# Optimization experiments

Hardware: AMD Instinct MI355X
Metric: run time of the kernel (lower is better)

Reference implementation:

```python
import jax, jax.numpy as jnp
import numpy as np

BETA = 0.9
THRESHOLD = 1.0

B, T, I, H, O = 64, 512, 256, 512, 256


def setup_inputs() -> dict:
    key = jax.random.key(0)
    ks = jax.random.split(key, 10)
    s_in = 1.0 / np.sqrt(I)
    s_h = 1.0 / np.sqrt(H)
    return {
        "x": jax.random.normal(ks[0], (B, T, I), dtype=jnp.float32),
        "W_in": jax.random.uniform(ks[1], (H, I), jnp.float32, -s_in, s_in),
        "b_in": jax.random.uniform(ks[2], (H,), jnp.float32, -s_in, s_in),
        "W_ih": jax.random.uniform(ks[3], (H, H), jnp.float32, -s_h, s_h),
        "b_ih": jax.random.uniform(ks[4], (H,), jnp.float32, -s_h, s_h),
        "W_hh": jax.random.uniform(ks[5], (H, H), jnp.float32, -s_h, s_h),
        "b_hh": jax.random.uniform(ks[6], (H,), jnp.float32, -s_h, s_h),
        "W_out": jax.random.uniform(ks[7], (O, H), jnp.float32, -s_h, s_h),
        "b_out": jax.random.uniform(ks[8], (O,), jnp.float32, -s_h, s_h),
        "temporal_attention": jax.random.normal(ks[9], (T, O), dtype=jnp.float32),
    }


def _lif(mem, cur):
    # LIF with 'subtract' reset: new_mem*(1-s) + s*(new_mem-thr) == new_mem - s*thr
    new_mem = BETA * mem + cur
    spike = (new_mem > THRESHOLD).astype(new_mem.dtype)
    return new_mem - spike * THRESHOLD, spike


def reference(x, W_in, b_in, W_ih, b_ih, W_hh, b_hh, W_out, b_out, temporal_attention):
    dtype = x.dtype
    batch, time_steps, _ = x.shape
    hidden = W_in.shape[0]

    # Input projection for all time steps at once: (B,T,H) -> scan over T.
    input_proj = jnp.einsum('bti,hi->tbh', x, W_in) + b_in  # (T,B,H)

    mem0 = jnp.zeros((batch, hidden), dtype=dtype)
    _, hidden_spikes = jax.lax.scan(_lif, mem0, input_proj)  # (T,B,H)

    # Recurrent layer: input->hidden projection precomputed; hidden->hidden uses
    # carried membrane potential (as in the torch module).
    in_proj = jnp.einsum('tbh,gh->tbg', hidden_spikes, W_ih) + b_ih  # (T,B,H)

    def rec_step(mem, ip):
        total = ip + mem @ W_hh.T + b_hh
        return _lif(mem, total)

    _, temporal_spikes = jax.lax.scan(rec_step, mem0, in_proj)  # (T,B,H)

    out_proj = jnp.einsum('tbh,oh->tbo', temporal_spikes, W_out) + b_out  # (T,B,O)

    attn = jax.nn.softmax(temporal_attention[:time_steps], axis=0)  # (T,O)
    attended = jnp.einsum('tbo,to->bo', out_proj, attn)  # (B,O)

    # Final LIF from zero membrane: new_mem = attended; spike = (attended > thr)
    final_spikes = (attended > THRESHOLD).astype(dtype)
    return final_spikes
```

## Files before the change

### kernel.cpp

```cpp
#include <hip/hip_runtime.h>
#include <hip/hip_bf16.h>
#include <cstdint>


#define T_STEPS 512
#define BATCH 64
#define HID 512
#define IN_DIM 256
#define OUT_DIM 256
#define BETA 0.9f
#define THR 1.0f
#define SENT 0x7FC00000u

typedef __attribute__((ext_vector_type(8))) short short8;
typedef __attribute__((ext_vector_type(4))) float float4v;
typedef unsigned short ushort_t;

__global__ __launch_bounds__(256) void k_fill_nan(uint32_t* __restrict__ P) {
  const int idx = blockIdx.x * 256 + threadIdx.x;
  uint4 s = make_uint4(SENT, SENT, SENT, SENT);
  uint4* p4 = (uint4*)P;
  for (int i = idx; i < (32768 * 512) / 4; i += 65536) p4[i] = s;
}

__global__ __launch_bounds__(256) void k_split(const float* __restrict__ src,
                                               ushort_t* __restrict__ hi,
                                               ushort_t* __restrict__ lo, int n) {
  int i = blockIdx.x * 256 + threadIdx.x;
  const int stride = gridDim.x * 256;
  for (; i < n; i += stride) {
    float v = src[i];
    uint32_t u = __float_as_uint(v);
    uint32_t rh = u + 0x7FFFu + ((u >> 16) & 1u);
    ushort_t h = (ushort_t)(rh >> 16);
    float hf = __uint_as_float(((uint32_t)h) << 16);
    float l = v - hf;
    uint32_t ul = __float_as_uint(l);
    uint32_t rl = ul + 0x7FFFu + ((ul >> 16) & 1u);
    hi[i] = h;
    lo[i] = (ushort_t)(rl >> 16);
  }
}

__global__ __launch_bounds__(256) void k_softmax_t(
    const float* __restrict__ TA, float* __restrict__ attn) {
  __shared__ float redm[8][32];
  __shared__ float reds[8][32];
  const int ol = threadIdx.x & 31;
  const int tg = threadIdx.x >> 5;
  const int o = blockIdx.x * 32 + ol;
  float mx = -1e30f;
  for (int i = 0; i < 64; ++i) {
    float v = TA[(size_t)(tg * 64 + i) * OUT_DIM + o];
    mx = fmaxf(mx, v);
  }
  redm[tg][ol] = mx;
  __syncthreads();
  float m = redm[0][ol];
#pragma unroll
  for (int j = 1; j < 8; ++j) m = fmaxf(m, redm[j][ol]);
  float s = 0.f;
  for (int i = 0; i < 64; ++i) {
    float v = TA[(size_t)(tg * 64 + i) * OUT_DIM + o];
    s += __expf(v - m);
  }
  reds[tg][ol] = s;
  __syncthreads();
  float tot = 0.f;
#pragma unroll
  for (int j = 0; j < 8; ++j) tot += reds[j][ol];
  const float inv = 1.0f / tot;
  for (int i = 0; i < 64; ++i) {
    int t = tg * 64 + i;
    float v = TA[(size_t)t * OUT_DIM + o];
    attn[(size_t)t * OUT_DIM + o] = __expf(v - m) * inv;
  }
}

__global__ __launch_bounds__(256) void k_gemm_split3(
    const ushort_t* __restrict__ Ahi, const ushort_t* __restrict__ Alo,
    const ushort_t* __restrict__ Bhi, const ushort_t* __restrict__ Blo,
    const float* __restrict__ bias, float* __restrict__ C,
    int M, int N, int K) {
  __shared__ ushort_t At[2][128 * 40];
  __shared__ ushort_t Bt[2][128 * 40];
  const int tid = threadIdx.x;
  const int row0 = blockIdx.x * 128, col0 = blockIdx.y * 128;
  const int w = tid >> 6, lane = tid & 63;
  const int wm = (w >> 1) * 64, wn = (w & 1) * 64;
  const int l15 = lane & 15, quad = lane >> 4;
  float4v acc[4][4];
#pragma unroll
  for (int i = 0; i < 4; ++i)
#pragma unroll
    for (int j = 0; j < 4; ++j) acc[i][j] = (float4v){0.f, 0.f, 0.f, 0.f};

  for (int k0 = 0; k0 < K; k0 += 32) {
#pragma unroll
    for (int it = 0; it < 2; ++it) {
      int idx = it * 256 + tid;
      int r = idx >> 2;
      int c8 = (idx & 3) << 3;
      *(uint4*)(&At[0][r * 40 + c8]) =
          *(const uint4*)(&Ahi[(size_t)(row0 + r) * K + k0 + c8]);
      *(uint4*)(&At[1][r * 40 + c8]) =
          *(const uint4*)(&Alo[(size_t)(row0 + r) * K + k0 + c8]);
      *(uint4*)(&Bt[0][r * 40 + c8]) =
          *(const uint4*)(&Bhi[(size_t)(col0 + r) * K + k0 + c8]);
      *(uint4*)(&Bt[1][r * 40 + c8]) =
          *(const uint4*)(&Blo[(size_t)(col0 + r) * K + k0 + c8]);
    }
    __syncthreads();
    short8 ah[4], al[4], bh[4], bl[4];
    const int koff = quad * 8;
#pragma unroll
    for (int i = 0; i < 4; ++i) {
      ah[i] = *(const short8*)(&At[0][(wm + i * 16 + l15) * 40 + koff]);
      al[i] = *(const short8*)(&At[1][(wm + i * 16 + l15) * 40 + koff]);
      bh[i] = *(const short8*)(&Bt[0][(wn + i * 16 + l15) * 40 + koff]);
      bl[i] = *(const short8*)(&Bt[1][(wn + i * 16 + l15) * 40 + koff]);
    }
#pragma unroll
    for (int i = 0; i < 4; ++i)
#pragma unroll
      for (int j = 0; j < 4; ++j) {
        acc[i][j] = __builtin_amdgcn_mfma_f32_16x16x32_bf16(ah[i], bh[j], acc[i][j], 0, 0, 0);
        acc[i][j] = __builtin_amdgcn_mfma_f32_16x16x32_bf16(ah[i], bl[j], acc[i][j], 0, 0, 0);
        acc[i][j] = __builtin_amdgcn_mfma_f32_16x16x32_bf16(al[i], bh[j], acc[i][j], 0, 0, 0);
      }
    __syncthreads();
  }
#pragma unroll
  for (int j = 0; j < 4; ++j) {
    const int col = col0 + wn + j * 16 + l15;
    const float bv = bias ? bias[col] : 0.f;
#pragma unroll
    for (int i = 0; i < 4; ++i) {
#pragma unroll
      for (int r = 0; r < 4; ++r) {
        int row = row0 + wm + i * 16 + quad * 4 + r;
        C[(size_t)row * N + col] = acc[i][j][r] + bv;
      }
    }
  }
}

__global__ __launch_bounds__(256) void k_gemm_spike2(
    const float* __restrict__ A, const ushort_t* __restrict__ Bhi,
    const ushort_t* __restrict__ Blo, const float* __restrict__ bias,
    float* __restrict__ C, int M, int N, int K) {
  __shared__ ushort_t At[128 * 72];
  __shared__ ushort_t Bt[2][128 * 72];
  const int tid = threadIdx.x;
  const int row0 = blockIdx.x * 128, col0 = blockIdx.y * 128;
  const int w = tid >> 6, lane = tid & 63;
  const int wm = (w >> 1) * 64, wn = (w & 1) * 64;
  const int l15 = lane & 15, quad = lane >> 4;
  float4v acc[4][4];
#pragma unroll
  for (int i = 0; i < 4; ++i)
#pragma unroll
    for (int j = 0; j < 4; ++j) acc[i][j] = (float4v){0.f, 0.f, 0.f, 0.f};

  for (int k0 = 0; k0 < K; k0 += 64) {
#pragma unroll
    for (int it = 0; it < 4; ++it) {
      int idx = it * 256 + tid;
      int r = idx >> 3;
      int c8 = (idx & 7) << 3;
      uint4 pa = *(const uint4*)(&A[(size_t)(row0 + r) * K + k0 + c8]);
      uint4 pb = *(const uint4*)(&A[(size_t)(row0 + r) * K + k0 + c8 + 4]);
      uint4 st;
      st.x = (pa.x >> 16) | (pa.y & 0xFFFF0000u);
      st.y = (pa.z >> 16) | (pa.w & 0xFFFF0000u);
      st.z = (pb.x >> 16) | (pb.y & 0xFFFF0000u);
      st.w = (pb.z >> 16) | (pb.w & 0xFFFF0000u);
      *(uint4*)(&At[r * 72 + c8]) = st;
      *(uint4*)(&Bt[0][r * 72 + c8]) =
          *(const uint4*)(&Bhi[(size_t)(col0 + r) * K + k0 + c8]);
      *(uint4*)(&Bt[1][r * 72 + c8]) =
          *(const uint4*)(&Blo[(size_t)(col0 + r) * K + k0 + c8]);
    }
    __syncthreads();
#pragma unroll
    for (int ks = 0; ks < 2; ++ks) {
      short8 a[4], bh[4], bl[4];
      const int koff = ks * 32 + quad * 8;
#pragma unroll
      for (int i = 0; i < 4; ++i) {
        a[i] = *(const short8*)(&At[(wm + i * 16 + l15) * 72 + koff]);
        bh[i] = *(const short8*)(&Bt[0][(wn + i * 16 + l15) * 72 + koff]);
        bl[i] = *(const short8*)(&Bt[1][(wn + i * 16 + l15) * 72 + koff]);
      }
#pragma unroll
      for (int i = 0; i < 4; ++i)
#pragma unroll
        for (int j = 0; j < 4; ++j) {
          acc[i][j] = __builtin_amdgcn_mfma_f32_16x16x32_bf16(a[i], bh[j], acc[i][j], 0, 0, 0);
          acc[i][j] = __builtin_amdgcn_mfma_f32_16x16x32_bf16(a[i], bl[j], acc[i][j], 0, 0, 0);
        }
    }
    __syncthreads();
  }
#pragma unroll
  for (int j = 0; j < 4; ++j) {
    const int col = col0 + wn + j * 16 + l15;
    const float bv = bias ? bias[col] : 0.f;
#pragma unroll
    for (int i = 0; i < 4; ++i) {
#pragma unroll
      for (int r = 0; r < 4; ++r) {
        int row = row0 + wm + i * 16 + quad * 4 + r;
        C[(size_t)row * N + col] = acc[i][j][r] + bv;
      }
    }
  }
}

__global__ __launch_bounds__(256) void k_lif1(float* __restrict__ p) {
  const int id = blockIdx.x * 256 + threadIdx.x;
  const size_t base = (size_t)(id >> 9) * (T_STEPS * HID) + (id & 511);
  float mem = 0.f;
  for (int t0 = 0; t0 < T_STEPS; t0 += 8) {
    float v[8];
#pragma unroll
    for (int j = 0; j < 8; ++j) v[j] = p[base + (size_t)(t0 + j) * HID];
#pragma unroll
    for (int j = 0; j < 8; ++j) {
      float nm = BETA * mem + v[j];
      float sp = nm > THR ? 1.0f : 0.0f;
      p[base + (size_t)(t0 + j) * HID] = sp;
      mem = nm - sp;
    }
  }
}

__global__ __launch_bounds__(512) void k_recurrent_cp(
    const float* __restrict__ W, const float* __restrict__ b_hh,
    float* __restrict__ rp, float* __restrict__ P) {
  const int tid = threadIdx.x;
  const int grp = blockIdx.x & 31;
  const int j   = blockIdx.x >> 5;
  const int w   = tid >> 6;
  const int l   = tid & 63;
  const int q   = l >> 3;
  const int c   = l & 7;
  const int row = (w << 3) + q;
  const int g0  = j << 6;

  __shared__ float memLDS[2][2][8 * 72];

  for (int i = tid; i < 2 * 2 * 8 * 72; i += 512) ((float*)memLDS)[i] = 0.f;

  float Wreg[64];
  {
    const float* wrow = W + (size_t)(g0 + row) * HID + (c << 6);
#pragma unroll
    for (int k4 = 0; k4 < 16; ++k4) {
      float4 w4 = *(const float4*)(wrow + 4 * k4);
      Wreg[4 * k4 + 0] = w4.x; Wreg[4 * k4 + 1] = w4.y;
      Wreg[4 * k4 + 2] = w4.z; Wreg[4 * k4 + 3] = w4.w;
    }
  }

  const bool lif = (c == 0);
  const int og = g0 + row;
  const size_t rp_b0 = (size_t)(grp * 2 + 0) * (T_STEPS * HID) + og;
  const size_t rp_b1 = (size_t)(grp * 2 + 1) * (T_STEPS * HID) + og;
  const float bhh_v = lif ? b_hh[og] : 0.f;
  float mem0 = 0.f, mem1 = 0.f;

  const int rg = (tid < g0) ? tid : tid + 64;
  const int raddr = (rg >> 6) * 72 + (rg & 63);

  const uint32_t* Pu = (const uint32_t*)P;
  float* Pf = P;

  __syncthreads();

  for (int t = 0; t < T_STEPS; ++t) {
    const int par = t & 1;
    float ip0 = 0.f, ip1 = 0.f;
    if (lif) {
      ip0 = rp[rp_b0 + (size_t)t * HID];
      ip1 = rp[rp_b1 + (size_t)t * HID];
    }
    if (t > 0 && tid < 448) {
      const size_t slot = ((size_t)(t - 1) * 32 + grp) * 1024;
      const uint32_t* a0p = Pu + slot + rg;
      const uint32_t* a1p = a0p + 512;
      uint32_t u0 = __hip_atomic_load(a0p, __ATOMIC_RELAXED, __HIP_MEMORY_SCOPE_AGENT);
      uint32_t u1 = __hip_atomic_load(a1p, __ATOMIC_RELAXED, __HIP_MEMORY_SCOPE_AGENT);
      if (u0 == SENT || u1 == SENT) {
        uint32_t v0 = __hip_atomic_load(a0p, __ATOMIC_RELAXED, __HIP_MEMORY_SCOPE_AGENT);
        uint32_t v1 = __hip_atomic_load(a1p, __ATOMIC_RELAXED, __HIP_MEMORY_SCOPE_AGENT);
        int tries = 0;
        do {
          uint32_t w0 = __hip_atomic_load(a0p, __ATOMIC_RELAXED, __HIP_MEMORY_SCOPE_AGENT);
          uint32_t w1 = __hip_atomic_load(a1p, __ATOMIC_RELAXED, __HIP_MEMORY_SCOPE_AGENT);
          if (u0 == SENT) u0 = v0;
          if (u1 == SENT) u1 = v1;
          v0 = w0; v1 = w1;
          if (++tries > 24) __builtin_amdgcn_s_sleep(1);
        } while (u0 == SENT || u1 == SENT);
      }
      memLDS[par][0][raddr] = __uint_as_float(u0);
      memLDS[par][1][raddr] = __uint_as_float(u1);
    }
    __syncthreads();

    float p0a = 0.f, p0b = 0.f, p1a = 0.f, p1b = 0.f;
    {
      const float4* m0 = (const float4*)&memLDS[par][0][c * 72];
      const float4* m1 = (const float4*)&memLDS[par][1][c * 72];
#pragma unroll
      for (int k4 = 0; k4 < 16; ++k4) {
        float4 a = m0[k4];
        float4 b = m1[k4];
        p0a = fmaf(Wreg[4 * k4 + 0], a.x, p0a);
        p0b = fmaf(Wreg[4 * k4 + 1], a.y, p0b);
        p0a = fmaf(Wreg[4 * k4 + 2], a.z, p0a);
        p0b = fmaf(Wreg[4 * k4 + 3], a.w, p0b);
        p1a = fmaf(Wreg[4 * k4 + 0], b.x, p1a);
        p1b = fmaf(Wreg[4 * k4 + 1], b.y, p1b);
        p1a = fmaf(Wreg[4 * k4 + 2], b.z, p1a);
        p1b = fmaf(Wreg[4 * k4 + 3], b.w, p1b);
      }
    }
    const int i0 = __float_as_int(p0a + p0b);
    const int i1 = __float_as_int(p1a + p1b);
    float s0 = 0.f, s1 = 0.f;
#define RED(ss)                                                                 \
    s0 += __int_as_float(__builtin_amdgcn_ds_swizzle(i0, ((ss) << 5) | 0x18)); \
    s1 += __int_as_float(__builtin_amdgcn_ds_swizzle(i1, ((ss) << 5) | 0x18));
    RED(0) RED(1) RED(2) RED(3) RED(4) RED(5) RED(6) RED(7)
#undef RED

    if (lif) {
      const int npar = par ^ 1;
      const size_t slot = ((size_t)t * 32 + grp) * 1024;
      const float nm0 = BETA * mem0 + ip0 + s0 + bhh_v;
      const float sp0 = nm0 > THR ? 1.0f : 0.0f;
      mem0 = nm0 - sp0;
      __hip_atomic_store(Pf + slot + og, mem0, __ATOMIC_RELAXED, __HIP_MEMORY_SCOPE_AGENT);
      const float nm1 = BETA * mem1 + ip1 + s1 + bhh_v;
      const float sp1 = nm1 > THR ? 1.0f : 0.0f;
      mem1 = nm1 - sp1;
      __hip_atomic_store(Pf + slot + 512 + og, mem1, __ATOMIC_RELAXED, __HIP_MEMORY_SCOPE_AGENT);
      rp[rp_b0 + (size_t)t * HID] = sp0;
      rp[rp_b1 + (size_t)t * HID] = sp1;
      memLDS[npar][0][j * 72 + row] = mem0;
      memLDS[npar][1][j * 72 + row] = mem1;
    }
  }
}

__global__ __launch_bounds__(256) void k_attend(
    const float* __restrict__ op, const float* __restrict__ attn,
    const float* __restrict__ b_out, float* __restrict__ out) {
  const int b = blockIdx.x;
  const int o = threadIdx.x;
  float s = b_out[o];
  const float* opb = op + (size_t)b * T_STEPS * OUT_DIM + o;
  for (int t0 = 0; t0 < T_STEPS; t0 += 8) {
    float av[8], pv[8];
#pragma unroll
    for (int j = 0; j < 8; ++j) {
      av[j] = attn[(size_t)(t0 + j) * OUT_DIM + o];
      pv[j] = opb[(size_t)(t0 + j) * OUT_DIM];
    }
#pragma unroll
    for (int j = 0; j < 8; ++j) s = fmaf(av[j], pv[j], s);
  }
  out[b * OUT_DIM + o] = s > THR ? 1.0f : 0.0f;
}

extern "C" void kernel_launch(void* const* d_in, const int* in_sizes, int n_in,
                              void* d_out, int out_size, void* d_ws, size_t ws_size,
                              hipStream_t stream) {
  (void)in_sizes; (void)n_in; (void)out_size; (void)ws_size;
  const float* x     = (const float*)d_in[0];
  const float* W_in  = (const float*)d_in[1];
  const float* b_in  = (const float*)d_in[2];
  const float* W_ih  = (const float*)d_in[3];
  const float* b_ih  = (const float*)d_in[4];
  const float* W_hh  = (const float*)d_in[5];
  const float* b_hh  = (const float*)d_in[6];
  const float* W_out = (const float*)d_in[7];
  const float* b_out = (const float*)d_in[8];
  const float* TA    = (const float*)d_in[9];

  float* ws = (float*)d_ws;
  float* proj  = ws;
  float* rproj = proj + (size_t)32768 * 512;
  float* attn  = rproj + (size_t)32768 * 512;
  ushort_t* wih_hi = (ushort_t*)(attn + 512 * 256);
  ushort_t* wih_lo = wih_hi + 512 * 512;
  ushort_t* win_hi = wih_lo + 512 * 512;
  ushort_t* win_lo = win_hi + 512 * 256;
  ushort_t* wout_hi = win_lo + 512 * 256;
  ushort_t* wout_lo = wout_hi + 256 * 512;
  ushort_t* x_hi = (ushort_t*)rproj;
  ushort_t* x_lo = x_hi + (size_t)32768 * 256;
  float* P = proj;
  float* out_proj = proj;

  k_softmax_t<<<8, 256, 0, stream>>>(TA, attn);
  k_split<<<4096, 256, 0, stream>>>(x, x_hi, x_lo, 32768 * 256);
  k_split<<<512, 256, 0, stream>>>(W_in, win_hi, win_lo, 512 * 256);
  k_split<<<512, 256, 0, stream>>>(W_ih, wih_hi, wih_lo, 512 * 512);
  k_split<<<512, 256, 0, stream>>>(W_out, wout_hi, wout_lo, 256 * 512);

  k_gemm_split3<<<dim3(256, 4), 256, 0, stream>>>(
      x_hi, x_lo, win_hi, win_lo, b_in, proj, 32768, 512, 256);
  k_lif1<<<128, 256, 0, stream>>>(proj);
  k_gemm_spike2<<<dim3(256, 4), 256, 0, stream>>>(
      proj, wih_hi, wih_lo, b_ih, rproj, 32768, 512, 512);
  k_fill_nan<<<256, 256, 0, stream>>>((uint32_t*)P);
  k_recurrent_cp<<<256, 512, 0, stream>>>(W_hh, b_hh, rproj, P);
  k_gemm_spike2<<<dim3(256, 2), 256, 0, stream>>>(
      rproj, wout_hi, wout_lo, nullptr, out_proj, 32768, 256, 512);
  k_attend<<<64, 256, 0, stream>>>(out_proj, attn, b_out, (float*)d_out);
}
```

Baseline: 1.049 ms.

## Give each wave a private LDS copy of memory state and drop block barriers

Each wavefront now loads the full previous-step membrane vector for both batches itself and keeps it in its own LDS slice. This removes the per-timestep __syncthreads and the block-local LDS forwarding. The two batch values are packed into one 64-bit word, so one atomic store and one atomic load carry a pair. The cost is roughly 8x more global loads per block per step, with every wave polling sentinels independently, in exchange for no block-wide barrier on the serial critical path.

```diff
diff --git a/kernel.cpp b/kernel.cpp
--- a/kernel.cpp
+++ b/kernel.cpp
@@ -248,9 +248,11 @@
   const int row = (w << 3) + q;
   const int g0  = j << 6;
 
-  __shared__ float memLDS[2][2][8 * 72];
-
-  for (int i = tid; i < 2 * 2 * 8 * 72; i += 512) ((float*)memLDS)[i] = 0.f;
+  __shared__ float memLDS[8][2][8 * 72];
+  float* wl0 = &memLDS[w][0][0];
+  float* wl1 = &memLDS[w][1][0];
+
+  for (int i = l; i < 2 * 8 * 72; i += 64) ((float*)memLDS[w])[i] = 0.f;
 
   float Wreg[64];
   {
@@ -270,49 +272,49 @@
   const float bhh_v = lif ? b_hh[og] : 0.f;
   float mem0 = 0.f, mem1 = 0.f;
 
-  const int rg = (tid < g0) ? tid : tid + 64;
-  const int raddr = (rg >> 6) * 72 + (rg & 63);
-
-  const uint32_t* Pu = (const uint32_t*)P;
-  float* Pf = P;
-
-  __syncthreads();
+  const uint64_t* P64 = (const uint64_t*)P;
+  uint64_t* P64w = (uint64_t*)P;
 
   for (int t = 0; t < T_STEPS; ++t) {
-    const int par = t & 1;
     float ip0 = 0.f, ip1 = 0.f;
     if (lif) {
       ip0 = rp[rp_b0 + (size_t)t * HID];
       ip1 = rp[rp_b1 + (size_t)t * HID];
     }
-    if (t > 0 && tid < 448) {
-      const size_t slot = ((size_t)(t - 1) * 32 + grp) * 1024;
-      const uint32_t* a0p = Pu + slot + rg;
-      const uint32_t* a1p = a0p + 512;
-      uint32_t u0 = __hip_atomic_load(a0p, __ATOMIC_RELAXED, __HIP_MEMORY_SCOPE_AGENT);
-      uint32_t u1 = __hip_atomic_load(a1p, __ATOMIC_RELAXED, __HIP_MEMORY_SCOPE_AGENT);
-      if (u0 == SENT || u1 == SENT) {
-        uint32_t v0 = __hip_atomic_load(a0p, __ATOMIC_RELAXED, __HIP_MEMORY_SCOPE_AGENT);
-        uint32_t v1 = __hip_atomic_load(a1p, __ATOMIC_RELAXED, __HIP_MEMORY_SCOPE_AGENT);
-        int tries = 0;
-        do {
-          uint32_t w0 = __hip_atomic_load(a0p, __ATOMIC_RELAXED, __HIP_MEMORY_SCOPE_AGENT);
-          uint32_t w1 = __hip_atomic_load(a1p, __ATOMIC_RELAXED, __HIP_MEMORY_SCOPE_AGENT);
-          if (u0 == SENT) u0 = v0;
-          if (u1 == SENT) u1 = v1;
-          v0 = w0; v1 = w1;
-          if (++tries > 24) __builtin_amdgcn_s_sleep(1);
-        } while (u0 == SENT || u1 == SENT);
-      }
-      memLDS[par][0][raddr] = __uint_as_float(u0);
-      memLDS[par][1][raddr] = __uint_as_float(u1);
-    }
-    __syncthreads();
+    if (t > 0) {
+      const uint64_t* base = P64 + ((size_t)(t - 1) * 32 + grp) * 512;
+      uint64_t u[8];
+#pragma unroll
+      for (int i = 0; i < 8; ++i)
+        u[i] = __hip_atomic_load(base + (i << 6) + l, __ATOMIC_RELAXED,
+                                 __HIP_MEMORY_SCOPE_AGENT);
+      int tries = 0;
+      for (;;) {
+        bool any = false;
+#pragma unroll
+        for (int i = 0; i < 8; ++i) {
+          any = any || ((uint32_t)u[i] == SENT) || ((uint32_t)(u[i] >> 32) == SENT);
+        }
+        if (!any) break;
+        if (++tries > 16) __builtin_amdgcn_s_sleep(1);
+#pragma unroll
+        for (int i = 0; i < 8; ++i) {
+          if (((uint32_t)u[i] == SENT) || ((uint32_t)(u[i] >> 32) == SENT))
+            u[i] = __hip_atomic_load(base + (i << 6) + l, __ATOMIC_RELAXED,
+                                     __HIP_MEMORY_SCOPE_AGENT);
+        }
+      }
+#pragma unroll
+      for (int i = 0; i < 8; ++i) {
+        wl0[i * 72 + l] = __uint_as_float((uint32_t)u[i]);
+        wl1[i * 72 + l] = __uint_as_float((uint32_t)(u[i] >> 32));
+      }
+    }
 
     float p0a = 0.f, p0b = 0.f, p1a = 0.f, p1b = 0.f;
     {
-      const float4* m0 = (const float4*)&memLDS[par][0][c * 72];
-      const float4* m1 = (const float4*)&memLDS[par][1][c * 72];
+      const float4* m0 = (const float4*)&wl0[c * 72];
+      const float4* m1 = (const float4*)&wl1[c * 72];
 #pragma unroll
       for (int k4 = 0; k4 < 16; ++k4) {
         float4 a = m0[k4];
@@ -337,20 +339,18 @@
 #undef RED
 
     if (lif) {
-      const int npar = par ^ 1;
-      const size_t slot = ((size_t)t * 32 + grp) * 1024;
       const float nm0 = BETA * mem0 + ip0 + s0 + bhh_v;
       const float sp0 = nm0 > THR ? 1.0f : 0.0f;
       mem0 = nm0 - sp0;
-      __hip_atomic_store(Pf + slot + og, mem0, __ATOMIC_RELAXED, __HIP_MEMORY_SCOPE_AGENT);
       const float nm1 = BETA * mem1 + ip1 + s1 + bhh_v;
       const float sp1 = nm1 > THR ? 1.0f : 0.0f;
       mem1 = nm1 - sp1;
-      __hip_atomic_store(Pf + slot + 512 + og, mem1, __ATOMIC_RELAXED, __HIP_MEMORY_SCOPE_AGENT);
+      const uint64_t pk =
+          ((uint64_t)__float_as_uint(mem1) << 32) | (uint64_t)__float_as_uint(mem0);
+      __hip_atomic_store(P64w + ((size_t)t * 32 + grp) * 512 + og, pk,
+                         __ATOMIC_RELAXED, __HIP_MEMORY_SCOPE_AGENT);
       rp[rp_b0 + (size_t)t * HID] = sp0;
       rp[rp_b1 + (size_t)t * HID] = sp1;
-      memLDS[npar][0][j * 72 + row] = mem0;
-      memLDS[npar][1][j * 72 + row] = mem1;
     }
   }
 }
```

Measured after the change: 1.778 ms. 1.7x slower.

## Replace NaN-sentinel exchange buffer with small self-validating ring buffers

Applied to the files above, without the earlier changes.

The full-size NaN-filled exchange buffer (64 MB fill) is replaced by two small ring buffers. One is a 4-deep ring of 16-byte entries that carry both membrane values, the step index and an XOR checksum, so a reader can validate an entry with one dwordx4 load. The other is an 8-deep ring of 64-bit sentinel-checked pairs, used as a fallback path, with a slot three steps ahead reset to the sentinel after each write. This removes the large fill kernel and makes polling traffic cache-friendly, at the cost of relying on 16-byte store atomicity and a hand-written asm load and wait, plus more writes per step.

```diff
diff --git a/kernel.cpp b/kernel.cpp
--- a/kernel.cpp
+++ b/kernel.cpp
@@ -11,16 +11,21 @@
 #define BETA 0.9f
 #define THR 1.0f
 #define SENT 0x7FC00000u
+#define RF 4
+#define RS 8
 
 typedef __attribute__((ext_vector_type(8))) short short8;
 typedef __attribute__((ext_vector_type(4))) float float4v;
+typedef __attribute__((ext_vector_type(4))) unsigned int uint32x4;
 typedef unsigned short ushort_t;
 
-__global__ __launch_bounds__(256) void k_fill_nan(uint32_t* __restrict__ P) {
+__global__ __launch_bounds__(256) void k_init_rings(uint32x4* __restrict__ FR,
+                                                    uint64_t* __restrict__ SR) {
   const int idx = blockIdx.x * 256 + threadIdx.x;
-  uint4 s = make_uint4(SENT, SENT, SENT, SENT);
-  uint4* p4 = (uint4*)P;
-  for (int i = idx; i < (32768 * 512) / 4; i += 65536) p4[i] = s;
+  FR[idx] = (uint32x4){0u, 0u, 0xFFFFFFFFu, 0u};
+  const uint64_t SP = ((uint64_t)SENT << 32) | (uint64_t)SENT;
+  SR[idx] = SP;
+  SR[idx + 65536] = SP;
 }
 
 __global__ __launch_bounds__(256) void k_split(const float* __restrict__ src,
@@ -237,7 +242,8 @@
 
 __global__ __launch_bounds__(512) void k_recurrent_cp(
     const float* __restrict__ W, const float* __restrict__ b_hh,
-    float* __restrict__ rp, float* __restrict__ P) {
+    float* __restrict__ rp, uint32x4* __restrict__ FR,
+    uint64_t* __restrict__ SR) {
   const int tid = threadIdx.x;
   const int grp = blockIdx.x & 31;
   const int j   = blockIdx.x >> 5;
@@ -272,9 +278,7 @@
 
   const int rg = (tid < g0) ? tid : tid + 64;
   const int raddr = (rg >> 6) * 72 + (rg & 63);
-
-  const uint32_t* Pu = (const uint32_t*)P;
-  float* Pf = P;
+  const uint64_t SENTP = ((uint64_t)SENT << 32) | (uint64_t)SENT;
 
   __syncthreads();
 
@@ -286,26 +290,27 @@
       ip1 = rp[rp_b1 + (size_t)t * HID];
     }
     if (t > 0 && tid < 448) {
-      const size_t slot = ((size_t)(t - 1) * 32 + grp) * 1024;
-      const uint32_t* a0p = Pu + slot + rg;
-      const uint32_t* a1p = a0p + 512;
-      uint32_t u0 = __hip_atomic_load(a0p, __ATOMIC_RELAXED, __HIP_MEMORY_SCOPE_AGENT);
-      uint32_t u1 = __hip_atomic_load(a1p, __ATOMIC_RELAXED, __HIP_MEMORY_SCOPE_AGENT);
-      if (u0 == SENT || u1 == SENT) {
-        uint32_t v0 = __hip_atomic_load(a0p, __ATOMIC_RELAXED, __HIP_MEMORY_SCOPE_AGENT);
-        uint32_t v1 = __hip_atomic_load(a1p, __ATOMIC_RELAXED, __HIP_MEMORY_SCOPE_AGENT);
-        int tries = 0;
-        do {
-          uint32_t w0 = __hip_atomic_load(a0p, __ATOMIC_RELAXED, __HIP_MEMORY_SCOPE_AGENT);
-          uint32_t w1 = __hip_atomic_load(a1p, __ATOMIC_RELAXED, __HIP_MEMORY_SCOPE_AGENT);
-          if (u0 == SENT) u0 = v0;
-          if (u1 == SENT) u1 = v1;
-          v0 = w0; v1 = w1;
-          if (++tries > 24) __builtin_amdgcn_s_sleep(1);
-        } while (u0 == SENT || u1 == SENT);
-      }
-      memLDS[par][0][raddr] = __uint_as_float(u0);
-      memLDS[par][1][raddr] = __uint_as_float(u1);
+      const uint32_t want = (uint32_t)(t - 1);
+      const uint32x4* fp_ = FR + (((size_t)((t - 1) & (RF - 1))) * 32 + grp) * 512 + rg;
+      const uint64_t* sp_ = SR + (((size_t)((t - 1) & (RS - 1))) * 32 + grp) * 512 + rg;
+      uint32_t r0, r1;
+      int tries = 0;
+      for (;;) {
+        uint32x4 fq;
+        asm volatile("global_load_dwordx4 %0, %1, off sc0"
+                     : "=v"(fq) : "v"(fp_) : "memory");
+        uint64_t sq = __hip_atomic_load(sp_, __ATOMIC_RELAXED,
+                                        __HIP_MEMORY_SCOPE_AGENT);
+        asm volatile("s_waitcnt vmcnt(1)" : "+v"(fq) :: "memory");
+        if (fq.z == want && fq.w == (want ^ fq.x ^ fq.y)) {
+          r0 = fq.x; r1 = fq.y; break;
+        }
+        const uint32_t s0 = (uint32_t)sq, s1 = (uint32_t)(sq >> 32);
+        if (s0 != SENT && s1 != SENT) { r0 = s0; r1 = s1; break; }
+        if (++tries > 48) __builtin_amdgcn_s_sleep(1);
+      }
+      memLDS[par][0][raddr] = __uint_as_float(r0);
+      memLDS[par][1][raddr] = __uint_as_float(r1);
     }
     __syncthreads();
 
@@ -338,15 +343,24 @@
 
     if (lif) {
       const int npar = par ^ 1;
-      const size_t slot = ((size_t)t * 32 + grp) * 1024;
       const float nm0 = BETA * mem0 + ip0 + s0 + bhh_v;
       const float sp0 = nm0 > THR ? 1.0f : 0.0f;
       mem0 = nm0 - sp0;
-      __hip_atomic_store(Pf + slot + og, mem0, __ATOMIC_RELAXED, __HIP_MEMORY_SCOPE_AGENT);
       const float nm1 = BETA * mem1 + ip1 + s1 + bhh_v;
       const float sp1 = nm1 > THR ? 1.0f : 0.0f;
       mem1 = nm1 - sp1;
-      __hip_atomic_store(Pf + slot + 512 + og, mem1, __ATOMIC_RELAXED, __HIP_MEMORY_SCOPE_AGENT);
+      const uint32_t w0 = __float_as_uint(mem0);
+      const uint32_t w1 = __float_as_uint(mem1);
+      uint32x4 e;
+      e.x = w0; e.y = w1; e.z = (uint32_t)t; e.w = (uint32_t)t ^ w0 ^ w1;
+      uint32x4* fo = FR + (((size_t)(t & (RF - 1))) * 32 + grp) * 512 + og;
+      asm volatile("global_store_dwordx4 %0, %1, off sc0"
+                   :: "v"(fo), "v"(e) : "memory");
+      const uint64_t pk = ((uint64_t)w1 << 32) | (uint64_t)w0;
+      __hip_atomic_store(SR + (((size_t)(t & (RS - 1))) * 32 + grp) * 512 + og,
+                         pk, __ATOMIC_RELAXED, __HIP_MEMORY_SCOPE_AGENT);
+      __hip_atomic_store(SR + (((size_t)((t + 3) & (RS - 1))) * 32 + grp) * 512 + og,
+                         SENTP, __ATOMIC_RELAXED, __HIP_MEMORY_SCOPE_AGENT);
       rp[rp_b0 + (size_t)t * HID] = sp0;
       rp[rp_b1 + (size_t)t * HID] = sp1;
       memLDS[npar][0][j * 72 + row] = mem0;
@@ -402,7 +416,8 @@
   ushort_t* wout_lo = wout_hi + 256 * 512;
   ushort_t* x_hi = (ushort_t*)rproj;
   ushort_t* x_lo = x_hi + (size_t)32768 * 256;
-  float* P = proj;
+  uint32x4* FR = (uint32x4*)proj;
+  uint64_t* SR = (uint64_t*)(proj + (size_t)262144);
   float* out_proj = proj;
 
   k_softmax_t<<<8, 256, 0, stream>>>(TA, attn);
@@ -416,8 +431,8 @@
   k_lif1<<<128, 256, 0, stream>>>(proj);
   k_gemm_spike2<<<dim3(256, 4), 256, 0, stream>>>(
       proj, wih_hi, wih_lo, b_ih, rproj, 32768, 512, 512);
-  k_fill_nan<<<256, 256, 0, stream>>>((uint32_t*)P);
-  k_recurrent_cp<<<256, 512, 0, stream>>>(W_hh, b_hh, rproj, P);
+  k_init_rings<<<256, 256, 0, stream>>>(FR, SR);
+  k_recurrent_cp<<<256, 512, 0, stream>>>(W_hh, b_hh, rproj, FR, SR);
   k_gemm_spike2<<<dim3(256, 2), 256, 0, stream>>>(
       rproj, wout_hi, wout_lo, nullptr, out_proj, 32768, 256, 512);
   k_attend<<<64, 256, 0, stream>>>(out_proj, attn, b_out, (float*)d_out);
```

Measured after the change: 1.336 ms. +27.4%, slower.

## Fuse x bf16 split into input GEMM and pack recurrent exchange into 64-bit atomics

Applied to the files above, without the earlier changes.

The separate split kernel that turned x into hi/lo bf16 arrays is removed. The input-projection GEMM now loads fp32 x directly and does the hi/lo rounding while staging tiles into LDS, which removes a full write and re-read of the split x arrays. Separately, the recurrent kernel's cross-block membrane exchange now stores both batch values as one 64-bit atomic and polls with a single 64-bit load, cutting the number of atomic operations on the serial critical path. The cost is that the GEMM does the rounding per column tile (four times per x element), and the exchange buffer layout changes.

```diff
diff --git a/kernel.cpp b/kernel.cpp
--- a/kernel.cpp
+++ b/kernel.cpp
@@ -15,6 +15,7 @@
 typedef __attribute__((ext_vector_type(8))) short short8;
 typedef __attribute__((ext_vector_type(4))) float float4v;
 typedef unsigned short ushort_t;
+typedef unsigned long long u64_t;
 
 __global__ __launch_bounds__(256) void k_fill_nan(uint32_t* __restrict__ P) {
   const int idx = blockIdx.x * 256 + threadIdx.x;
@@ -42,6 +43,22 @@
   }
 }
 
+__device__ __forceinline__ uint32_t rne_hi2(uint32_t ua, uint32_t ub) {
+  uint32_t ra = ua + 0x7FFFu + ((ua >> 16) & 1u);
+  uint32_t rb = ub + 0x7FFFu + ((ub >> 16) & 1u);
+  return (ra >> 16) | (rb & 0xFFFF0000u);
+}
+__device__ __forceinline__ uint32_t rne_lo2(uint32_t ua, uint32_t ub) {
+  uint32_t ra = ua + 0x7FFFu + ((ua >> 16) & 1u);
+  uint32_t rb = ub + 0x7FFFu + ((ub >> 16) & 1u);
+  float la = __uint_as_float(ua) - __uint_as_float(ra & 0xFFFF0000u);
+  float lb = __uint_as_float(ub) - __uint_as_float(rb & 0xFFFF0000u);
+  uint32_t ula = __float_as_uint(la), ulb = __float_as_uint(lb);
+  uint32_t rla = ula + 0x7FFFu + ((ula >> 16) & 1u);
+  uint32_t rlb = ulb + 0x7FFFu + ((ulb >> 16) & 1u);
+  return (rla >> 16) | (rlb & 0xFFFF0000u);
+}
+
 __global__ __launch_bounds__(256) void k_softmax_t(
     const float* __restrict__ TA, float* __restrict__ attn) {
   __shared__ float redm[8][32];
@@ -77,11 +94,10 @@
   }
 }
 
-__global__ __launch_bounds__(256) void k_gemm_split3(
-    const ushort_t* __restrict__ Ahi, const ushort_t* __restrict__ Alo,
-    const ushort_t* __restrict__ Bhi, const ushort_t* __restrict__ Blo,
-    const float* __restrict__ bias, float* __restrict__ C,
-    int M, int N, int K) {
+__global__ __launch_bounds__(256) void k_gemm_fsplit3(
+    const float* __restrict__ A, const ushort_t* __restrict__ Bhi,
+    const ushort_t* __restrict__ Blo, const float* __restrict__ bias,
+    float* __restrict__ C, int M, int N, int K) {
   __shared__ ushort_t At[2][128 * 40];
   __shared__ ushort_t Bt[2][128 * 40];
   const int tid = threadIdx.x;
@@ -101,10 +117,16 @@
       int idx = it * 256 + tid;
       int r = idx >> 2;
       int c8 = (idx & 3) << 3;
-      *(uint4*)(&At[0][r * 40 + c8]) =
-          *(const uint4*)(&Ahi[(size_t)(row0 + r) * K + k0 + c8]);
-      *(uint4*)(&At[1][r * 40 + c8]) =
-          *(const uint4*)(&Alo[(size_t)(row0 + r) * K + k0 + c8]);
+      const float* ap_ = &A[(size_t)(row0 + r) * K + k0 + c8];
+      uint4 f0 = *(const uint4*)ap_;
+      uint4 f1 = *(const uint4*)(ap_ + 4);
+      uint4 hi4, lo4;
+      hi4.x = rne_hi2(f0.x, f0.y); lo4.x = rne_lo2(f0.x, f0.y);
+      hi4.y = rne_hi2(f0.z, f0.w); lo4.y = rne_lo2(f0.z, f0.w);
+      hi4.z = rne_hi2(f1.x, f1.y); lo4.z = rne_lo2(f1.x, f1.y);
+      hi4.w = rne_hi2(f1.z, f1.w); lo4.w = rne_lo2(f1.z, f1.w);
+      *(uint4*)(&At[0][r * 40 + c8]) = hi4;
+      *(uint4*)(&At[1][r * 40 + c8]) = lo4;
       *(uint4*)(&Bt[0][r * 40 + c8]) =
           *(const uint4*)(&Bhi[(size_t)(col0 + r) * K + k0 + c8]);
       *(uint4*)(&Bt[1][r * 40 + c8]) =
@@ -273,8 +295,7 @@
   const int rg = (tid < g0) ? tid : tid + 64;
   const int raddr = (rg >> 6) * 72 + (rg & 63);
 
-  const uint32_t* Pu = (const uint32_t*)P;
-  float* Pf = P;
+  u64_t* Pq = (u64_t*)P;
 
   __syncthreads();
 
@@ -286,26 +307,15 @@
       ip1 = rp[rp_b1 + (size_t)t * HID];
     }
     if (t > 0 && tid < 448) {
-      const size_t slot = ((size_t)(t - 1) * 32 + grp) * 1024;
-      const uint32_t* a0p = Pu + slot + rg;
-      const uint32_t* a1p = a0p + 512;
-      uint32_t u0 = __hip_atomic_load(a0p, __ATOMIC_RELAXED, __HIP_MEMORY_SCOPE_AGENT);
-      uint32_t u1 = __hip_atomic_load(a1p, __ATOMIC_RELAXED, __HIP_MEMORY_SCOPE_AGENT);
-      if (u0 == SENT || u1 == SENT) {
-        uint32_t v0 = __hip_atomic_load(a0p, __ATOMIC_RELAXED, __HIP_MEMORY_SCOPE_AGENT);
-        uint32_t v1 = __hip_atomic_load(a1p, __ATOMIC_RELAXED, __HIP_MEMORY_SCOPE_AGENT);
-        int tries = 0;
-        do {
-          uint32_t w0 = __hip_atomic_load(a0p, __ATOMIC_RELAXED, __HIP_MEMORY_SCOPE_AGENT);
-          uint32_t w1 = __hip_atomic_load(a1p, __ATOMIC_RELAXED, __HIP_MEMORY_SCOPE_AGENT);
-          if (u0 == SENT) u0 = v0;
-          if (u1 == SENT) u1 = v1;
-          v0 = w0; v1 = w1;
-          if (++tries > 24) __builtin_amdgcn_s_sleep(1);
-        } while (u0 == SENT || u1 == SENT);
-      }
-      memLDS[par][0][raddr] = __uint_as_float(u0);
-      memLDS[par][1][raddr] = __uint_as_float(u1);
+      const u64_t* ap = Pq + ((size_t)(t - 1) * 32 + grp) * 512 + rg;
+      u64_t u = __hip_atomic_load(ap, __ATOMIC_RELAXED, __HIP_MEMORY_SCOPE_AGENT);
+      int tries = 0;
+      while (((uint32_t)u == SENT) || ((uint32_t)(u >> 32) == SENT)) {
+        if (++tries > 24) __builtin_amdgcn_s_sleep(1);
+        u = __hip_atomic_load(ap, __ATOMIC_RELAXED, __HIP_MEMORY_SCOPE_AGENT);
+      }
+      memLDS[par][0][raddr] = __uint_as_float((uint32_t)u);
+      memLDS[par][1][raddr] = __uint_as_float((uint32_t)(u >> 32));
     }
     __syncthreads();
 
@@ -338,15 +348,16 @@
 
     if (lif) {
       const int npar = par ^ 1;
-      const size_t slot = ((size_t)t * 32 + grp) * 1024;
       const float nm0 = BETA * mem0 + ip0 + s0 + bhh_v;
       const float sp0 = nm0 > THR ? 1.0f : 0.0f;
       mem0 = nm0 - sp0;
-      __hip_atomic_store(Pf + slot + og, mem0, __ATOMIC_RELAXED, __HIP_MEMORY_SCOPE_AGENT);
       const float nm1 = BETA * mem1 + ip1 + s1 + bhh_v;
       const float sp1 = nm1 > THR ? 1.0f : 0.0f;
       mem1 = nm1 - sp1;
-      __hip_atomic_store(Pf + slot + 512 + og, mem1, __ATOMIC_RELAXED, __HIP_MEMORY_SCOPE_AGENT);
+      const u64_t pk =
+          ((u64_t)__float_as_uint(mem1) << 32) | (u64_t)__float_as_uint(mem0);
+      __hip_atomic_store(Pq + ((size_t)t * 32 + grp) * 512 + og, pk,
+                         __ATOMIC_RELAXED, __HIP_MEMORY_SCOPE_AGENT);
       rp[rp_b0 + (size_t)t * HID] = sp0;
       rp[rp_b1 + (size_t)t * HID] = sp1;
       memLDS[npar][0][j * 72 + row] = mem0;
@@ -400,19 +411,16 @@
   ushort_t* win_lo = win_hi + 512 * 256;
   ushort_t* wout_hi = win_lo + 512 * 256;
   ushort_t* wout_lo = wout_hi + 256 * 512;
-  ushort_t* x_hi = (ushort_t*)rproj;
-  ushort_t* x_lo = x_hi + (size_t)32768 * 256;
   float* P = proj;
   float* out_proj = proj;
 
   k_softmax_t<<<8, 256, 0, stream>>>(TA, attn);
-  k_split<<<4096, 256, 0, stream>>>(x, x_hi, x_lo, 32768 * 256);
   k_split<<<512, 256, 0, stream>>>(W_in, win_hi, win_lo, 512 * 256);
   k_split<<<512, 256, 0, stream>>>(W_ih, wih_hi, wih_lo, 512 * 512);
   k_split<<<512, 256, 0, stream>>>(W_out, wout_hi, wout_lo, 256 * 512);
 
-  k_gemm_split3<<<dim3(256, 4), 256, 0, stream>>>(
-      x_hi, x_lo, win_hi, win_lo, b_in, proj, 32768, 512, 256);
+  k_gemm_fsplit3<<<dim3(256, 4), 256, 0, stream>>>(
+      x, win_hi, win_lo, b_in, proj, 32768, 512, 256);
   k_lif1<<<128, 256, 0, stream>>>(proj);
   k_gemm_spike2<<<dim3(256, 4), 256, 0, stream>>>(
       proj, wih_hi, wih_lo, b_ih, rproj, 32768, 512, 512);
```

Result: faster. 990.1 us (-5.6%).
